# Optimization experiments

Hardware: AMD Instinct MI355X
Metric: run time of the kernel (lower is better)

Reference implementation:

```python
import jax, jax.numpy as jnp
import numpy as np

NUM_GRAPHS = 4096
EPS = 1e-6

def _ln(x, g, b):
    mu = jnp.mean(x, axis=-1, keepdims=True)
    var = jnp.mean(jnp.square(x - mu), axis=-1, keepdims=True)
    return (x - mu) * jax.lax.rsqrt(var + EPS) * g + b

def setup_inputs() -> dict:
    key = jax.random.key(0)
    ks = jax.random.split(key, 8)
    N, D, H, DRUG = 262144, 128, 8, 128
    feat = jax.random.normal(ks[0], (N, D), dtype=jnp.float32)
    batch = jnp.sort(jax.random.randint(ks[1], (N,), 0, NUM_GRAPHS)).astype(jnp.int64)
    def lin(k, fi, fo):
        lim = 1.0 / np.sqrt(fi)
        return jax.random.uniform(k, (fi, fo), jnp.float32, -lim, lim)
    return {
        'feat': feat, 'batch': batch,
        'W1': lin(ks[2], D, 64), 'b1': jnp.zeros((64,), jnp.float32),
        'g1': jnp.ones((64,), jnp.float32), 'beta1': jnp.zeros((64,), jnp.float32),
        'W2': lin(ks[3], 64, H), 'b2': jnp.zeros((H,), jnp.float32),
        'W3': lin(ks[4], H * D, D), 'b3': jnp.zeros((D,), jnp.float32),
        'g3': jnp.ones((D,), jnp.float32), 'beta3': jnp.zeros((D,), jnp.float32),
        'W4': lin(ks[5], D, DRUG), 'b4': jnp.zeros((DRUG,), jnp.float32),
        'g4': jnp.ones((DRUG,), jnp.float32), 'beta4': jnp.zeros((DRUG,), jnp.float32),
    }

def reference(feat, batch, W1, b1, g1, beta1, W2, b2, W3, b3, g3, beta3, W4, b4, g4, beta4):
    seg = batch.astype(jnp.int32)
    # ATFC: Linear -> LeakyReLU -> LayerNorm -> Linear
    h = jax.nn.leaky_relu(feat @ W1 + b1)
    h = _ln(h, g1, beta1)
    att = jnp.exp(h @ W2 + b2)                      # [N, H]
    # segment softmax normalization
    s = jax.ops.segment_sum(att, seg, num_segments=NUM_GRAPHS)  # [B, H]
    att = att / s[seg]
    # weighted aggregation: outer product + segment sum -> [B, H, D]
    out = jax.ops.segment_sum(att[:, :, None] * feat[:, None, :], seg, num_segments=NUM_GRAPHS)
    out = out.reshape(NUM_GRAPHS, -1)               # [B, H*D]
    # output block (dropout is identity in eval mode)
    o = _ln(jax.nn.leaky_relu(out @ W3 + b3), g3, beta3)
    o = _ln(jax.nn.leaky_relu(o @ W4 + b4), g4, beta4)
    return o
```

## Files before the change

kernel.cpp:

```cpp
#include <hip/hip_runtime.h>
#include <math.h>

#define NG 4096
#define NN 262144
#define D 128
#define M1 64
#define NH 8
#define GPB 8
#define EPS 1e-6f

typedef __attribute__((ext_vector_type(8))) short short8;
typedef __attribute__((ext_vector_type(8))) unsigned char uchar8;
typedef __attribute__((ext_vector_type(4))) float f32x4;

__device__ inline float leaky(float x) { return x > 0.f ? x : 0.01f * x; }

__device__ inline short f2bf(float f) {
  union { float f; unsigned u; } v; v.f = f;
  unsigned r = (v.u + 0x7fffu + ((v.u >> 16) & 1u)) >> 16;
  return (short)r;
}
__device__ inline float bf2f(short s) {
  union { unsigned u; float f; } v;
  v.u = ((unsigned)(unsigned short)s) << 16;
  return v.f;
}

__global__ __launch_bounds__(256) void k0b_prep(
    const float* __restrict__ W3, const float* __restrict__ W4,
    const int* __restrict__ batch,
    short* __restrict__ W3T, short* __restrict__ W4T,
    int* __restrict__ starts) {
  __shared__ float tile[64][65];
  int b = blockIdx.x, t = threadIdx.x;
  if (b >= 36) {
    int g = (b - 36) * 256 + t;
    int lo = 0, hi = NN;
    while (lo < hi) {
      int mid = (lo + hi) >> 1;
      if (batch[mid] < g) lo = mid + 1; else hi = mid;
    }
    starts[g] = lo;
    if (g == 0) starts[NG] = NN;
    return;
  }
  const float* src; short* dst; int kt, nt, tkl;
  if (b < 32) { src = W3; dst = W3T; kt = b >> 1; nt = b & 1; tkl = 1024; }
  else        { src = W4; dst = W4T; kt = (b - 32) >> 1; nt = (b - 32) & 1; tkl = 128; }

#pragma unroll
  for (int i = 0; i < 4; ++i) {
    int id = t + 256 * i;
    int r = id >> 4, c4 = (id & 15) * 4;
    float4 v = *(const float4*)(src + (size_t)(kt * 64 + r) * D + nt * 64 + c4);
    tile[r][c4 + 0] = v.x; tile[r][c4 + 1] = v.y;
    tile[r][c4 + 2] = v.z; tile[r][c4 + 3] = v.w;
  }
  __syncthreads();
  int n = t >> 2, kb = (t & 3) * 16;
  short8 p0, p1;
#pragma unroll
  for (int j = 0; j < 8; ++j) {
    p0[j] = f2bf(tile[kb + j][n]);
    p1[j] = f2bf(tile[kb + 8 + j][n]);
  }
  short* o = dst + (size_t)(nt * 64 + n) * tkl + kt * 64 + kb;
  *(short8*)o = p0;
  *(short8*)(o + 8) = p1;
}

__global__ __launch_bounds__(256, 2) void k_fused(
    const float* __restrict__ feat, const int* __restrict__ batch,
    const int* __restrict__ starts,
    const float* __restrict__ W1, const float* __restrict__ b1,
    const float* __restrict__ g1, const float* __restrict__ beta1,
    const float* __restrict__ W2, const float* __restrict__ b2,
    const short* __restrict__ W3T, const float* __restrict__ b3,
    const float* __restrict__ g3, const float* __restrict__ beta3,
    const short* __restrict__ W4T, const float* __restrict__ b4,
    const float* __restrict__ g4, const float* __restrict__ beta4,
    float* __restrict__ out) {
  __shared__ short W1T[M1][D + 8];
  __shared__ short W2T[16][M1 + 8];
  __shared__ short hb[128][72];
  __shared__ float agg[GPB][NH][D + 4];
  __shared__ float sL[GPB][NH];
  __shared__ unsigned char giL2[2][128];
  __shared__ float red[4][2][16];
  __shared__ short hbuf2[16][136];

  short (*attB)[136] = (short(*)[136])&hb[0][0];
  short (*aL)[1040] = (short(*)[1040])&hb[0][0];

  int t = threadIdx.x;
  int G0 = blockIdx.x * GPB;
  int w = t >> 6, l = t & 63;
  int lr = l & 15, lq = l >> 4;

#pragma unroll
  for (int i = 0; i < 8; ++i) {
    int idx4 = t + 256 * i;
    int k = idx4 >> 4, j = (idx4 & 15) * 4;
    float4 wv = *(const float4*)(W1 + k * M1 + j);
    W1T[j + 0][k] = f2bf(wv.x);
    W1T[j + 1][k] = f2bf(wv.y);
    W1T[j + 2][k] = f2bf(wv.z);
    W1T[j + 3][k] = f2bf(wv.w);
  }
#pragma unroll
  for (int i = 0; i < 4; ++i) {
    int e = t * 4 + i;
    int hh = e >> 6, j = e & 63;
    W2T[hh][j] = (hh < NH) ? f2bf(W2[j * NH + hh]) : (short)0;
  }
  for (int i = t; i < GPB * NH * (D + 4); i += 256) (&agg[0][0][0])[i] = 0.f;
  if (t < GPB * NH) (&sL[0][0])[t] = 0.f;

  float b1v[4], g1v[4], btv[4];
#pragma unroll
  for (int nt = 0; nt < 4; ++nt) {
    b1v[nt] = b1[nt * 16 + lr];
    g1v[nt] = g1[nt * 16 + lr];
    btv[nt] = beta1[nt * 16 + lr];
  }
  float b2v = b2[lr & 7];

  int s0 = starts[G0], s1 = starts[G0 + GPB];
  int nchunks = (s1 - s0 + 127) >> 7;

  for (int c = 0; c < nchunks; ++c) {
    int base = s0 + (c << 7);
    int nvalid = min(128, s1 - base);
    unsigned char* gi = giL2[c & 1];
    if (t < 128)
      gi[t] = (t < nvalid) ? (unsigned char)(batch[base + t] - G0)
                           : (unsigned char)255;

    short8 afr[2][4];
#pragma unroll
    for (int mt = 0; mt < 2; ++mt) {
      int node = base + w * 32 + mt * 16 + lr;
      node = node < NN ? node : NN - 1;
      const float* rp = feat + (size_t)node * D + lq * 8;
#pragma unroll
      for (int cc = 0; cc < 4; ++cc) {
        float4 x0 = *(const float4*)(rp + cc * 32);
        float4 x1 = *(const float4*)(rp + cc * 32 + 4);
        short8 a;
        a[0] = f2bf(x0.x); a[1] = f2bf(x0.y); a[2] = f2bf(x0.z); a[3] = f2bf(x0.w);
        a[4] = f2bf(x1.x); a[5] = f2bf(x1.y); a[6] = f2bf(x1.z); a[7] = f2bf(x1.w);
        afr[mt][cc] = a;
      }
    }
    __syncthreads();

    f32x4 acc[2][4];
#pragma unroll
    for (int mt = 0; mt < 2; ++mt)
#pragma unroll
      for (int nt = 0; nt < 4; ++nt) acc[mt][nt] = (f32x4){0.f, 0.f, 0.f, 0.f};
#pragma unroll
    for (int cc = 0; cc < 4; ++cc) {
#pragma unroll
      for (int nt = 0; nt < 4; ++nt) {
        short8 bfr = *(const short8*)&W1T[nt * 16 + lr][cc * 32 + lq * 8];
        acc[0][nt] = __builtin_amdgcn_mfma_f32_16x16x32_bf16(afr[0][cc], bfr, acc[0][nt], 0, 0, 0);
        acc[1][nt] = __builtin_amdgcn_mfma_f32_16x16x32_bf16(afr[1][cc], bfr, acc[1][nt], 0, 0, 0);
      }
    }

#pragma unroll
    for (int mt = 0; mt < 2; ++mt) {
#pragma unroll
      for (int r = 0; r < 4; ++r) {
        float x[4], sa = 0.f, sb = 0.f;
#pragma unroll
        for (int nt = 0; nt < 4; ++nt) {
          float xvv = leaky(acc[mt][nt][r] + b1v[nt]);
          x[nt] = xvv; sa += xvv; sb = fmaf(xvv, xvv, sb);
        }
#pragma unroll
        for (int off = 1; off < 16; off <<= 1) {
          sa += __shfl_xor(sa, off);
          sb += __shfl_xor(sb, off);
        }
        float mu = sa * (1.f / M1);
        float var = sb * (1.f / M1) - mu * mu;
        float inv = rsqrtf(var + EPS);
        int node = w * 32 + mt * 16 + lq * 4 + r;
#pragma unroll
        for (int nt = 0; nt < 4; ++nt)
          hb[node][nt * 16 + lr] = f2bf((x[nt] - mu) * inv * g1v[nt] + btv[nt]);
      }
    }
    __syncthreads();

    f32x4 acc2[2];
    acc2[0] = (f32x4){0.f, 0.f, 0.f, 0.f};
    acc2[1] = (f32x4){0.f, 0.f, 0.f, 0.f};
#pragma unroll
    for (int c2 = 0; c2 < 2; ++c2) {
      short8 bfr2 = *(const short8*)&W2T[lr][c2 * 32 + lq * 8];
#pragma unroll
      for (int mt = 0; mt < 2; ++mt) {
        short8 af2 = *(const short8*)&hb[w * 32 + mt * 16 + lr][c2 * 32 + lq * 8];
        acc2[mt] = __builtin_amdgcn_mfma_f32_16x16x32_bf16(af2, bfr2, acc2[mt], 0, 0, 0);
      }
    }
    __syncthreads();

    int gl_lo = gi[0];
    int gl_hi = gi[nvalid - 1];

    if (lr < NH) {
      float attv[2][4];
      int gnode[2][4];
#pragma unroll
      for (int mt = 0; mt < 2; ++mt)
#pragma unroll
        for (int r = 0; r < 4; ++r) {
          int node = w * 32 + mt * 16 + lq * 4 + r;
          float av = bf2f(f2bf(expf(acc2[mt][r] + b2v)));
          attv[mt][r] = av;
          gnode[mt][r] = gi[node];
          attB[lr][node] = f2bf(av);
        }
      for (int g = gl_lo; g <= gl_hi; ++g) {
        float ss = 0.f;
#pragma unroll
        for (int mt = 0; mt < 2; ++mt)
#pragma unroll
          for (int r = 0; r < 4; ++r)
            ss += (gnode[mt][r] == g) ? attv[mt][r] : 0.f;
        ss += __shfl_xor(ss, 16);
        ss += __shfl_xor(ss, 32);
        if (lq == 0) atomicAdd(&sL[g][lr], ss);
      }
    }
    __syncthreads();

    int dA = w * 32 + lr, dB = dA + 16;
    short8 bfA[4], bfB[4];
#pragma unroll
    for (int kc = 0; kc < 4; ++kc) {
      short8 ba, bb;
#pragma unroll
      for (int j = 0; j < 8; ++j) {
        int node = base + kc * 32 + lq * 8 + j;
        node = node < NN ? node : NN - 1;
        const float* fp = feat + (size_t)node * D;
        ba[j] = f2bf(fp[dA]);
        bb[j] = f2bf(fp[dB]);
      }
      bfA[kc] = ba;
      bfB[kc] = bb;
    }

    int hA = lr & 7;
    for (int gp = gl_lo; gp <= gl_hi; gp += 4) {
      int t0 = gp + (lr >> 3);
      int t1 = t0 + 2;
      f32x4 c00 = (f32x4){0.f, 0.f, 0.f, 0.f};
      f32x4 c01 = (f32x4){0.f, 0.f, 0.f, 0.f};
      f32x4 c10 = (f32x4){0.f, 0.f, 0.f, 0.f};
      f32x4 c11 = (f32x4){0.f, 0.f, 0.f, 0.f};
#pragma unroll
      for (int kc = 0; kc < 4; ++kc) {
        short8 av = *(const short8*)&attB[hA][kc * 32 + lq * 8];
        uchar8 gv = *(const uchar8*)&gi[kc * 32 + lq * 8];
        short8 a0, a1;
#pragma unroll
        for (int j = 0; j < 8; ++j) {
          short x = av[j];
          a0[j] = (gv[j] == t0) ? x : (short)0;
          a1[j] = (gv[j] == t1) ? x : (short)0;
        }
        c00 = __builtin_amdgcn_mfma_f32_16x16x32_bf16(a0, bfA[kc], c00, 0, 0, 0);
        c01 = __builtin_amdgcn_mfma_f32_16x16x32_bf16(a0, bfB[kc], c01, 0, 0, 0);
        c10 = __builtin_amdgcn_mfma_f32_16x16x32_bf16(a1, bfA[kc], c10, 0, 0, 0);
        c11 = __builtin_amdgcn_mfma_f32_16x16x32_bf16(a1, bfB[kc], c11, 0, 0, 0);
      }
      int giC0 = gp + (lq >> 1);
      int giC1 = giC0 + 2;
      int hC = (lq & 1) * 4;
      if (giC0 < GPB) {
#pragma unroll
        for (int r = 0; r < 4; ++r) {
          agg[giC0][hC + r][dA] += c00[r];
          agg[giC0][hC + r][dB] += c01[r];
        }
      }
      if (giC1 < GPB) {
#pragma unroll
        for (int r = 0; r < 4; ++r) {
          agg[giC1][hC + r][dA] += c10[r];
          agg[giC1][hC + r][dB] += c11[r];
        }
      }
    }
  }
  __syncthreads();

  if (t < GPB * NH) {
    float sv = (&sL[0][0])[t];
    (&sL[0][0])[t] = sv > 0.f ? 1.f / sv : 0.f;
  }
  __syncthreads();

  for (int i = t; i < GPB * NH * D; i += 256) {
    int gi2 = i >> 10;
    int k = i & 1023;
    int h = k >> 7, d = k & 127;
    aL[gi2][k] = f2bf(agg[gi2][h][d] * sL[gi2][h]);
  }
  __syncthreads();

  int ar = lr & 7;
  f32x4 acc3[2];
  acc3[0] = (f32x4){0.f, 0.f, 0.f, 0.f};
  acc3[1] = (f32x4){0.f, 0.f, 0.f, 0.f};
#pragma unroll
  for (int kc = 0; kc < 32; ++kc) {
    short8 a = *(const short8*)&aL[ar][kc * 32 + lq * 8];
#pragma unroll
    for (int nt = 0; nt < 2; ++nt) {
      int ncol = w * 32 + nt * 16 + lr;
      short8 b = *(const short8*)(W3T + (size_t)ncol * 1024 + kc * 32 + lq * 8);
      acc3[nt] = __builtin_amdgcn_mfma_f32_16x16x32_bf16(a, b, acc3[nt], 0, 0, 0);
    }
  }

  float xv[2][4], sa[4] = {0.f, 0.f, 0.f, 0.f}, sb[4] = {0.f, 0.f, 0.f, 0.f};
#pragma unroll
  for (int nt = 0; nt < 2; ++nt) {
    float bb = b3[w * 32 + nt * 16 + lr];
#pragma unroll
    for (int r = 0; r < 4; ++r) {
      float v = leaky(acc3[nt][r] + bb);
      xv[nt][r] = v;
      sa[r] += v;
      sb[r] = fmaf(v, v, sb[r]);
    }
  }
#pragma unroll
  for (int off = 1; off < 16; off <<= 1)
#pragma unroll
    for (int r = 0; r < 4; ++r) {
      sa[r] += __shfl_xor(sa[r], off);
      sb[r] += __shfl_xor(sb[r], off);
    }
  if (lr == 0)
#pragma unroll
    for (int r = 0; r < 4; ++r) {
      red[w][0][lq * 4 + r] = sa[r];
      red[w][1][lq * 4 + r] = sb[r];
    }
  __syncthreads();
#pragma unroll
  for (int nt = 0; nt < 2; ++nt) {
    int col = w * 32 + nt * 16 + lr;
    float gg = g3[col], bt = beta3[col];
#pragma unroll
    for (int r = 0; r < 4; ++r) {
      int row = lq * 4 + r;
      float S1 = red[0][0][row] + red[1][0][row] + red[2][0][row] + red[3][0][row];
      float S2 = red[0][1][row] + red[1][1][row] + red[2][1][row] + red[3][1][row];
      float mu = S1 * (1.f / D);
      float var = S2 * (1.f / D) - mu * mu;
      float inv = rsqrtf(var + EPS);
      hbuf2[row][col] = f2bf((xv[nt][r] - mu) * inv * gg + bt);
    }
  }
  __syncthreads();

  f32x4 acc4[2];
  acc4[0] = (f32x4){0.f, 0.f, 0.f, 0.f};
  acc4[1] = (f32x4){0.f, 0.f, 0.f, 0.f};
#pragma unroll
  for (int kc = 0; kc < 4; ++kc) {
    short8 a2 = *(const short8*)&hbuf2[lr][kc * 32 + lq * 8];
#pragma unroll
    for (int nt = 0; nt < 2; ++nt) {
      int ncol = w * 32 + nt * 16 + lr;
      short8 b4f = *(const short8*)(W4T + (size_t)ncol * 128 + kc * 32 + lq * 8);
      acc4[nt] = __builtin_amdgcn_mfma_f32_16x16x32_bf16(a2, b4f, acc4[nt], 0, 0, 0);
    }
  }
#pragma unroll
  for (int r = 0; r < 4; ++r) { sa[r] = 0.f; sb[r] = 0.f; }
#pragma unroll
  for (int nt = 0; nt < 2; ++nt) {
    float bb = b4[w * 32 + nt * 16 + lr];
#pragma unroll
    for (int r = 0; r < 4; ++r) {
      float v = leaky(acc4[nt][r] + bb);
      xv[nt][r] = v;
      sa[r] += v;
      sb[r] = fmaf(v, v, sb[r]);
    }
  }
#pragma unroll
  for (int off = 1; off < 16; off <<= 1)
#pragma unroll
    for (int r = 0; r < 4; ++r) {
      sa[r] += __shfl_xor(sa[r], off);
      sb[r] += __shfl_xor(sb[r], off);
    }
  if (lr == 0)
#pragma unroll
    for (int r = 0; r < 4; ++r) {
      red[w][0][lq * 4 + r] = sa[r];
      red[w][1][lq * 4 + r] = sb[r];
    }
  __syncthreads();
#pragma unroll
  for (int nt = 0; nt < 2; ++nt) {
    int col = w * 32 + nt * 16 + lr;
    float gg = g4[col], bt = beta4[col];
#pragma unroll
    for (int r = 0; r < 4; ++r) {
      int row = lq * 4 + r;
      if (row < GPB) {
        float S1 = red[0][0][row] + red[1][0][row] + red[2][0][row] + red[3][0][row];
        float S2 = red[0][1][row] + red[1][1][row] + red[2][1][row] + red[3][1][row];
        float mu = S1 * (1.f / D);
        float var = S2 * (1.f / D) - mu * mu;
        float inv = rsqrtf(var + EPS);
        out[(size_t)(G0 + row) * D + col] = (xv[nt][r] - mu) * inv * gg + bt;
      }
    }
  }
}

extern "C" void kernel_launch(void* const* d_in, const int* in_sizes, int n_in,
                              void* d_out, int out_size, void* d_ws, size_t ws_size,
                              hipStream_t stream) {
  (void)in_sizes; (void)n_in; (void)out_size; (void)ws_size;
  const float* feat  = (const float*)d_in[0];
  const int*   batch = (const int*)d_in[1];
  const float* W1    = (const float*)d_in[2];
  const float* b1    = (const float*)d_in[3];
  const float* g1    = (const float*)d_in[4];
  const float* beta1 = (const float*)d_in[5];
  const float* W2    = (const float*)d_in[6];
  const float* b2    = (const float*)d_in[7];
  const float* W3    = (const float*)d_in[8];
  const float* b3    = (const float*)d_in[9];
  const float* g3    = (const float*)d_in[10];
  const float* beta3 = (const float*)d_in[11];
  const float* W4    = (const float*)d_in[12];
  const float* b4    = (const float*)d_in[13];
  const float* g4    = (const float*)d_in[14];
  const float* beta4 = (const float*)d_in[15];
  float* out = (float*)d_out;

  char* ws = (char*)d_ws;
  short* W3T   = (short*)ws;
  short* W4T   = (short*)(ws + 262144);
  int*  starts = (int*)(ws + 262144 + 32768);

  k0b_prep<<<52, 256, 0, stream>>>(W3, W4, batch, W3T, W4T, starts);
  k_fused<<<NG / GPB, 256, 0, stream>>>(feat, batch, starts, W1, b1, g1, beta1,
                                        W2, b2, W3T, b3, g3, beta3, W4T, b4, g4,
                                        beta4, out);
}
```

Measured before the change: 268.0 us.

## Halve graphs per block, keep aggregation in MFMA registers, overlay shared memory

Each block now handles 4 graphs instead of 8, so the segment-aggregation accumulators fit in four persistent MFMA register tiles across chunks. This removes the large shared-memory agg buffer and its read-modify-write traffic. Weight tiles and epilogue buffers share one shared-memory union, the strided feature gather is moved earlier to overlap the first matmul, and s_setprio hints are added around the MFMA loops. Launch bounds rise to 4 blocks per CU to raise occupancy, at the cost of twice as many blocks and more register pressure.

```diff
diff --git a/kernel.cpp b/kernel.cpp
--- a/kernel.cpp
+++ b/kernel.cpp
@@ -6,7 +6,7 @@
 #define D 128
 #define M1 64
 #define NH 8
-#define GPB 8
+#define GPB 4
 #define EPS 1e-6f
 
 typedef __attribute__((ext_vector_type(8))) short short8;
@@ -69,7 +69,7 @@
   *(short8*)(o + 8) = p1;
 }
 
-__global__ __launch_bounds__(256, 2) void k_fused(
+__global__ __launch_bounds__(256, 4) void k_fused(
     const float* __restrict__ feat, const int* __restrict__ batch,
     const int* __restrict__ starts,
     const float* __restrict__ W1, const float* __restrict__ b1,
@@ -80,40 +80,39 @@
     const short* __restrict__ W4T, const float* __restrict__ b4,
     const float* __restrict__ g4, const float* __restrict__ beta4,
     float* __restrict__ out) {
-  __shared__ short W1T[M1][D + 8];
-  __shared__ short W2T[16][M1 + 8];
-  __shared__ short hb[128][72];
-  __shared__ float agg[GPB][NH][D + 4];
+  __shared__ __align__(16) union SOvl {
+    struct { short W1T[M1][D + 8]; short W2T[16][M1 + 8]; } p;
+    struct { short hbuf2[16][136]; float red[4][2][16]; } e;
+  } ovl;
+  __shared__ __align__(16) short hb[128][72];
+  __shared__ __align__(16) short attB[NH][136];
   __shared__ float sL[GPB][NH];
   __shared__ unsigned char giL2[2][128];
-  __shared__ float red[4][2][16];
-  __shared__ short hbuf2[16][136];
-
-  short (*attB)[136] = (short(*)[136])&hb[0][0];
+
   short (*aL)[1040] = (short(*)[1040])&hb[0][0];
 
   int t = threadIdx.x;
   int G0 = blockIdx.x * GPB;
   int w = t >> 6, l = t & 63;
   int lr = l & 15, lq = l >> 4;
+  int dA = w * 32 + lr, dB = dA + 16;
 
 #pragma unroll
   for (int i = 0; i < 8; ++i) {
     int idx4 = t + 256 * i;
     int k = idx4 >> 4, j = (idx4 & 15) * 4;
     float4 wv = *(const float4*)(W1 + k * M1 + j);
-    W1T[j + 0][k] = f2bf(wv.x);
-    W1T[j + 1][k] = f2bf(wv.y);
-    W1T[j + 2][k] = f2bf(wv.z);
-    W1T[j + 3][k] = f2bf(wv.w);
+    ovl.p.W1T[j + 0][k] = f2bf(wv.x);
+    ovl.p.W1T[j + 1][k] = f2bf(wv.y);
+    ovl.p.W1T[j + 2][k] = f2bf(wv.z);
+    ovl.p.W1T[j + 3][k] = f2bf(wv.w);
   }
 #pragma unroll
   for (int i = 0; i < 4; ++i) {
     int e = t * 4 + i;
     int hh = e >> 6, j = e & 63;
-    W2T[hh][j] = (hh < NH) ? f2bf(W2[j * NH + hh]) : (short)0;
-  }
-  for (int i = t; i < GPB * NH * (D + 4); i += 256) (&agg[0][0][0])[i] = 0.f;
+    ovl.p.W2T[hh][j] = (hh < NH) ? f2bf(W2[j * NH + hh]) : (short)0;
+  }
   if (t < GPB * NH) (&sL[0][0])[t] = 0.f;
 
   float b1v[4], g1v[4], btv[4];
@@ -124,6 +123,11 @@
     btv[nt] = beta1[nt * 16 + lr];
   }
   float b2v = b2[lr & 7];
+
+  f32x4 c00 = (f32x4){0.f, 0.f, 0.f, 0.f};
+  f32x4 c01 = (f32x4){0.f, 0.f, 0.f, 0.f};
+  f32x4 c10 = (f32x4){0.f, 0.f, 0.f, 0.f};
+  f32x4 c11 = (f32x4){0.f, 0.f, 0.f, 0.f};
 
   int s0 = starts[G0], s1 = starts[G0 + GPB];
   int nchunks = (s1 - s0 + 127) >> 7;
@@ -152,6 +156,21 @@
         afr[mt][cc] = a;
       }
     }
+    short8 bfA[4], bfB[4];
+#pragma unroll
+    for (int kc = 0; kc < 4; ++kc) {
+      short8 ba, bb;
+#pragma unroll
+      for (int j = 0; j < 8; ++j) {
+        int node = base + kc * 32 + lq * 8 + j;
+        node = node < NN ? node : NN - 1;
+        const float* fp = feat + (size_t)node * D;
+        ba[j] = f2bf(fp[dA]);
+        bb[j] = f2bf(fp[dB]);
+      }
+      bfA[kc] = ba;
+      bfB[kc] = bb;
+    }
     __syncthreads();
 
     f32x4 acc[2][4];
@@ -159,15 +178,17 @@
     for (int mt = 0; mt < 2; ++mt)
 #pragma unroll
       for (int nt = 0; nt < 4; ++nt) acc[mt][nt] = (f32x4){0.f, 0.f, 0.f, 0.f};
+    __builtin_amdgcn_s_setprio(1);
 #pragma unroll
     for (int cc = 0; cc < 4; ++cc) {
 #pragma unroll
       for (int nt = 0; nt < 4; ++nt) {
-        short8 bfr = *(const short8*)&W1T[nt * 16 + lr][cc * 32 + lq * 8];
+        short8 bfr = *(const short8*)&ovl.p.W1T[nt * 16 + lr][cc * 32 + lq * 8];
         acc[0][nt] = __builtin_amdgcn_mfma_f32_16x16x32_bf16(afr[0][cc], bfr, acc[0][nt], 0, 0, 0);
         acc[1][nt] = __builtin_amdgcn_mfma_f32_16x16x32_bf16(afr[1][cc], bfr, acc[1][nt], 0, 0, 0);
       }
     }
+    __builtin_amdgcn_s_setprio(0);
 
 #pragma unroll
     for (int mt = 0; mt < 2; ++mt) {
@@ -200,14 +221,13 @@
     acc2[1] = (f32x4){0.f, 0.f, 0.f, 0.f};
 #pragma unroll
     for (int c2 = 0; c2 < 2; ++c2) {
-      short8 bfr2 = *(const short8*)&W2T[lr][c2 * 32 + lq * 8];
+      short8 bfr2 = *(const short8*)&ovl.p.W2T[lr][c2 * 32 + lq * 8];
 #pragma unroll
       for (int mt = 0; mt < 2; ++mt) {
         short8 af2 = *(const short8*)&hb[w * 32 + mt * 16 + lr][c2 * 32 + lq * 8];
         acc2[mt] = __builtin_amdgcn_mfma_f32_16x16x32_bf16(af2, bfr2, acc2[mt], 0, 0, 0);
       }
     }
-    __syncthreads();
 
     int gl_lo = gi[0];
     int gl_hi = gi[nvalid - 1];
@@ -239,65 +259,33 @@
     }
     __syncthreads();
 
-    int dA = w * 32 + lr, dB = dA + 16;
-    short8 bfA[4], bfB[4];
+    int hA = lr & 7;
+    int t0 = lr >> 3;
+    int t1 = t0 + 2;
+    __builtin_amdgcn_s_setprio(1);
 #pragma unroll
     for (int kc = 0; kc < 4; ++kc) {
-      short8 ba, bb;
-#pragma unroll
-      for (int j = 0; j < 8; ++j) {
-        int node = base + kc * 32 + lq * 8 + j;
-        node = node < NN ? node : NN - 1;
-        const float* fp = feat + (size_t)node * D;
-        ba[j] = f2bf(fp[dA]);
-        bb[j] = f2bf(fp[dB]);
-      }
-      bfA[kc] = ba;
-      bfB[kc] = bb;
-    }
-
-    int hA = lr & 7;
-    for (int gp = gl_lo; gp <= gl_hi; gp += 4) {
-      int t0 = gp + (lr >> 3);
-      int t1 = t0 + 2;
-      f32x4 c00 = (f32x4){0.f, 0.f, 0.f, 0.f};
-      f32x4 c01 = (f32x4){0.f, 0.f, 0.f, 0.f};
-      f32x4 c10 = (f32x4){0.f, 0.f, 0.f, 0.f};
-      f32x4 c11 = (f32x4){0.f, 0.f, 0.f, 0.f};
-#pragma unroll
-      for (int kc = 0; kc < 4; ++kc) {
-        short8 av = *(const short8*)&attB[hA][kc * 32 + lq * 8];
-        uchar8 gv = *(const uchar8*)&gi[kc * 32 + lq * 8];
-        short8 a0, a1;
-#pragma unroll
-        for (int j = 0; j < 8; ++j) {
-          short x = av[j];
-          a0[j] = (gv[j] == t0) ? x : (short)0;
-          a1[j] = (gv[j] == t1) ? x : (short)0;
-        }
+      int lo0 = gi[kc * 32];
+      if (lo0 > 3) continue;
+      int hi0 = gi[kc * 32 + 31];
+      short8 av = *(const short8*)&attB[hA][kc * 32 + lq * 8];
+      uchar8 gv = *(const uchar8*)&gi[kc * 32 + lq * 8];
+      if (lo0 <= 1) {
+        short8 a0;
+#pragma unroll
+        for (int j = 0; j < 8; ++j) a0[j] = (gv[j] == t0) ? av[j] : (short)0;
         c00 = __builtin_amdgcn_mfma_f32_16x16x32_bf16(a0, bfA[kc], c00, 0, 0, 0);
         c01 = __builtin_amdgcn_mfma_f32_16x16x32_bf16(a0, bfB[kc], c01, 0, 0, 0);
+      }
+      if (hi0 >= 2) {
+        short8 a1;
+#pragma unroll
+        for (int j = 0; j < 8; ++j) a1[j] = (gv[j] == t1) ? av[j] : (short)0;
         c10 = __builtin_amdgcn_mfma_f32_16x16x32_bf16(a1, bfA[kc], c10, 0, 0, 0);
         c11 = __builtin_amdgcn_mfma_f32_16x16x32_bf16(a1, bfB[kc], c11, 0, 0, 0);
       }
-      int giC0 = gp + (lq >> 1);
-      int giC1 = giC0 + 2;
-      int hC = (lq & 1) * 4;
-      if (giC0 < GPB) {
-#pragma unroll
-        for (int r = 0; r < 4; ++r) {
-          agg[giC0][hC + r][dA] += c00[r];
-          agg[giC0][hC + r][dB] += c01[r];
-        }
-      }
-      if (giC1 < GPB) {
-#pragma unroll
-        for (int r = 0; r < 4; ++r) {
-          agg[giC1][hC + r][dA] += c10[r];
-          agg[giC1][hC + r][dB] += c11[r];
-        }
-      }
-    }
+    }
+    __builtin_amdgcn_s_setprio(0);
   }
   __syncthreads();
 
@@ -307,15 +295,21 @@
   }
   __syncthreads();
 
-  for (int i = t; i < GPB * NH * D; i += 256) {
-    int gi2 = i >> 10;
-    int k = i & 1023;
-    int h = k >> 7, d = k & 127;
-    aL[gi2][k] = f2bf(agg[gi2][h][d] * sL[gi2][h]);
-  }
-  __syncthreads();
-
-  int ar = lr & 7;
+  {
+    int g0 = lq >> 1, g1i = g0 + 2;
+    int hC = (lq & 1) * 4;
+#pragma unroll
+    for (int r = 0; r < 4; ++r) {
+      float i0 = sL[g0][hC + r], i1 = sL[g1i][hC + r];
+      aL[g0][(hC + r) * 128 + dA] = f2bf(c00[r] * i0);
+      aL[g0][(hC + r) * 128 + dB] = f2bf(c01[r] * i0);
+      aL[g1i][(hC + r) * 128 + dA] = f2bf(c10[r] * i1);
+      aL[g1i][(hC + r) * 128 + dB] = f2bf(c11[r] * i1);
+    }
+  }
+  __syncthreads();
+
+  int ar = lr & 3;
   f32x4 acc3[2];
   acc3[0] = (f32x4){0.f, 0.f, 0.f, 0.f};
   acc3[1] = (f32x4){0.f, 0.f, 0.f, 0.f};
@@ -352,8 +346,8 @@
   if (lr == 0)
 #pragma unroll
     for (int r = 0; r < 4; ++r) {
-      red[w][0][lq * 4 + r] = sa[r];
-      red[w][1][lq * 4 + r] = sb[r];
+      ovl.e.red[w][0][lq * 4 + r] = sa[r];
+      ovl.e.red[w][1][lq * 4 + r] = sb[r];
     }
   __syncthreads();
 #pragma unroll
@@ -363,12 +357,14 @@
 #pragma unroll
     for (int r = 0; r < 4; ++r) {
       int row = lq * 4 + r;
-      float S1 = red[0][0][row] + red[1][0][row] + red[2][0][row] + red[3][0][row];
-      float S2 = red[0][1][row] + red[1][1][row] + red[2][1][row] + red[3][1][row];
+      float S1 = ovl.e.red[0][0][row] + ovl.e.red[1][0][row] +
+                 ovl.e.red[2][0][row] + ovl.e.red[3][0][row];
+      float S2 = ovl.e.red[0][1][row] + ovl.e.red[1][1][row] +
+                 ovl.e.red[2][1][row] + ovl.e.red[3][1][row];
       float mu = S1 * (1.f / D);
       float var = S2 * (1.f / D) - mu * mu;
       float inv = rsqrtf(var + EPS);
-      hbuf2[row][col] = f2bf((xv[nt][r] - mu) * inv * gg + bt);
+      ovl.e.hbuf2[row][col] = f2bf((xv[nt][r] - mu) * inv * gg + bt);
     }
   }
   __syncthreads();
@@ -378,7 +374,7 @@
   acc4[1] = (f32x4){0.f, 0.f, 0.f, 0.f};
 #pragma unroll
   for (int kc = 0; kc < 4; ++kc) {
-    short8 a2 = *(const short8*)&hbuf2[lr][kc * 32 + lq * 8];
+    short8 a2 = *(const short8*)&ovl.e.hbuf2[lr][kc * 32 + lq * 8];
 #pragma unroll
     for (int nt = 0; nt < 2; ++nt) {
       int ncol = w * 32 + nt * 16 + lr;
@@ -406,11 +402,12 @@
       sa[r] += __shfl_xor(sa[r], off);
       sb[r] += __shfl_xor(sb[r], off);
     }
+  __syncthreads();
   if (lr == 0)
 #pragma unroll
     for (int r = 0; r < 4; ++r) {
-      red[w][0][lq * 4 + r] = sa[r];
-      red[w][1][lq * 4 + r] = sb[r];
+      ovl.e.red[w][0][lq * 4 + r] = sa[r];
+      ovl.e.red[w][1][lq * 4 + r] = sb[r];
     }
   __syncthreads();
 #pragma unroll
@@ -421,8 +418,10 @@
     for (int r = 0; r < 4; ++r) {
       int row = lq * 4 + r;
       if (row < GPB) {
-        float S1 = red[0][0][row] + red[1][0][row] + red[2][0][row] + red[3][0][row];
-        float S2 = red[0][1][row] + red[1][1][row] + red[2][1][row] + red[3][1][row];
+        float S1 = ovl.e.red[0][0][row] + ovl.e.red[1][0][row] +
+                   ovl.e.red[2][0][row] + ovl.e.red[3][0][row];
+        float S2 = ovl.e.red[0][1][row] + ovl.e.red[1][1][row] +
+                   ovl.e.red[2][1][row] + ovl.e.red[3][1][row];
         float mu = S1 * (1.f / D);
         float var = S2 * (1.f / D) - mu * mu;
         float inv = rsqrtf(var + EPS);
```

Result: slower. 385.2 us (+43.8%).

## Split fused kernel into node-parallel attention and graph-parallel aggregation kernels

Applied to the files above, without the earlier changes.

The single fused kernel is split in two. The first is node-parallel, with one block per 128 nodes: it computes the attention logits, writes bf16 attention transposed to global memory, and atomically accumulates per-graph softmax sums. The second is graph-parallel: it re-reads feat and attention to build the per-graph aggregation with masked MFMA accumulators kept in registers rather than LDS atomics, then runs the output MLP. This removes the serial per-block chunk loop and the LDS agg buffer, which should improve occupancy, but it reads feat twice, adds global atomics and a memset, and adds an extra launch.

```diff
diff --git a/kernel.cpp b/kernel.cpp
--- a/kernel.cpp
+++ b/kernel.cpp
@@ -10,7 +10,7 @@
 #define EPS 1e-6f
 
 typedef __attribute__((ext_vector_type(8))) short short8;
-typedef __attribute__((ext_vector_type(8))) unsigned char uchar8;
+typedef __attribute__((ext_vector_type(4))) short short4v;
 typedef __attribute__((ext_vector_type(4))) float f32x4;
 
 __device__ inline float leaky(float x) { return x > 0.f ? x : 0.01f * x; }
@@ -69,31 +69,20 @@
   *(short8*)(o + 8) = p1;
 }
 
-__global__ __launch_bounds__(256, 2) void k_fused(
+__global__ __launch_bounds__(256, 2) void kA_att(
     const float* __restrict__ feat, const int* __restrict__ batch,
-    const int* __restrict__ starts,
     const float* __restrict__ W1, const float* __restrict__ b1,
     const float* __restrict__ g1, const float* __restrict__ beta1,
     const float* __restrict__ W2, const float* __restrict__ b2,
-    const short* __restrict__ W3T, const float* __restrict__ b3,
-    const float* __restrict__ g3, const float* __restrict__ beta3,
-    const short* __restrict__ W4T, const float* __restrict__ b4,
-    const float* __restrict__ g4, const float* __restrict__ beta4,
-    float* __restrict__ out) {
-  __shared__ short W1T[M1][D + 8];
-  __shared__ short W2T[16][M1 + 8];
-  __shared__ short hb[128][72];
-  __shared__ float agg[GPB][NH][D + 4];
-  __shared__ float sL[GPB][NH];
-  __shared__ unsigned char giL2[2][128];
-  __shared__ float red[4][2][16];
-  __shared__ short hbuf2[16][136];
-
-  short (*attB)[136] = (short(*)[136])&hb[0][0];
-  short (*aL)[1040] = (short(*)[1040])&hb[0][0];
+    short* __restrict__ attT, float* __restrict__ s_sum) {
+  __shared__ __align__(16) short W1T[M1][D + 8];
+  __shared__ __align__(16) short W2T[16][M1 + 8];
+  __shared__ __align__(16) short hb[128][72];
+  __shared__ __align__(16) short attB[NH][136];
+  __shared__ int batchL[128];
 
   int t = threadIdx.x;
-  int G0 = blockIdx.x * GPB;
+  int nb = blockIdx.x * 128;
   int w = t >> 6, l = t & 63;
   int lr = l & 15, lq = l >> 4;
 
@@ -113,8 +102,7 @@
     int hh = e >> 6, j = e & 63;
     W2T[hh][j] = (hh < NH) ? f2bf(W2[j * NH + hh]) : (short)0;
   }
-  for (int i = t; i < GPB * NH * (D + 4); i += 256) (&agg[0][0][0])[i] = 0.f;
-  if (t < GPB * NH) (&sL[0][0])[t] = 0.f;
+  if (t < 128) batchL[t] = batch[nb + t];
 
   float b1v[4], g1v[4], btv[4];
 #pragma unroll
@@ -125,193 +113,216 @@
   }
   float b2v = b2[lr & 7];
 
+  short8 afr[2][4];
+#pragma unroll
+  for (int mt = 0; mt < 2; ++mt) {
+    const float* rp = feat + (size_t)(nb + w * 32 + mt * 16 + lr) * D + lq * 8;
+#pragma unroll
+    for (int cc = 0; cc < 4; ++cc) {
+      float4 x0 = *(const float4*)(rp + cc * 32);
+      float4 x1 = *(const float4*)(rp + cc * 32 + 4);
+      short8 a;
+      a[0] = f2bf(x0.x); a[1] = f2bf(x0.y); a[2] = f2bf(x0.z); a[3] = f2bf(x0.w);
+      a[4] = f2bf(x1.x); a[5] = f2bf(x1.y); a[6] = f2bf(x1.z); a[7] = f2bf(x1.w);
+      afr[mt][cc] = a;
+    }
+  }
+  __syncthreads();
+
+  f32x4 acc[2][4];
+#pragma unroll
+  for (int mt = 0; mt < 2; ++mt)
+#pragma unroll
+    for (int nt = 0; nt < 4; ++nt) acc[mt][nt] = (f32x4){0.f, 0.f, 0.f, 0.f};
+  __builtin_amdgcn_s_setprio(1);
+#pragma unroll
+  for (int cc = 0; cc < 4; ++cc) {
+#pragma unroll
+    for (int nt = 0; nt < 4; ++nt) {
+      short8 bfr = *(const short8*)&W1T[nt * 16 + lr][cc * 32 + lq * 8];
+      acc[0][nt] = __builtin_amdgcn_mfma_f32_16x16x32_bf16(afr[0][cc], bfr, acc[0][nt], 0, 0, 0);
+      acc[1][nt] = __builtin_amdgcn_mfma_f32_16x16x32_bf16(afr[1][cc], bfr, acc[1][nt], 0, 0, 0);
+    }
+  }
+  __builtin_amdgcn_s_setprio(0);
+
+#pragma unroll
+  for (int mt = 0; mt < 2; ++mt) {
+#pragma unroll
+    for (int r = 0; r < 4; ++r) {
+      float x[4], sa = 0.f, sb = 0.f;
+#pragma unroll
+      for (int nt = 0; nt < 4; ++nt) {
+        float xvv = leaky(acc[mt][nt][r] + b1v[nt]);
+        x[nt] = xvv; sa += xvv; sb = fmaf(xvv, xvv, sb);
+      }
+#pragma unroll
+      for (int off = 1; off < 16; off <<= 1) {
+        sa += __shfl_xor(sa, off);
+        sb += __shfl_xor(sb, off);
+      }
+      float mu = sa * (1.f / M1);
+      float var = sb * (1.f / M1) - mu * mu;
+      float inv = rsqrtf(var + EPS);
+      int node = w * 32 + mt * 16 + lq * 4 + r;
+#pragma unroll
+      for (int nt = 0; nt < 4; ++nt)
+        hb[node][nt * 16 + lr] = f2bf((x[nt] - mu) * inv * g1v[nt] + btv[nt]);
+    }
+  }
+  __syncthreads();
+
+  f32x4 acc2[2];
+  acc2[0] = (f32x4){0.f, 0.f, 0.f, 0.f};
+  acc2[1] = (f32x4){0.f, 0.f, 0.f, 0.f};
+#pragma unroll
+  for (int c2 = 0; c2 < 2; ++c2) {
+    short8 bfr2 = *(const short8*)&W2T[lr][c2 * 32 + lq * 8];
+#pragma unroll
+    for (int mt = 0; mt < 2; ++mt) {
+      short8 af2 = *(const short8*)&hb[w * 32 + mt * 16 + lr][c2 * 32 + lq * 8];
+      acc2[mt] = __builtin_amdgcn_mfma_f32_16x16x32_bf16(af2, bfr2, acc2[mt], 0, 0, 0);
+    }
+  }
+
+  int g_lo = batchL[0], g_hi = batchL[127];
+
+  if (lr < NH) {
+    float attv[2][4];
+    int bnode[2][4];
+#pragma unroll
+    for (int mt = 0; mt < 2; ++mt)
+#pragma unroll
+      for (int r = 0; r < 4; ++r) {
+        int node = w * 32 + mt * 16 + lq * 4 + r;
+        float av = bf2f(f2bf(expf(acc2[mt][r] + b2v)));
+        attv[mt][r] = av;
+        bnode[mt][r] = batchL[node];
+        attB[lr][node] = f2bf(av);
+      }
+    for (int g = g_lo; g <= g_hi; ++g) {
+      float ss = 0.f;
+#pragma unroll
+      for (int mt = 0; mt < 2; ++mt)
+#pragma unroll
+        for (int r = 0; r < 4; ++r)
+          ss += (bnode[mt][r] == g) ? attv[mt][r] : 0.f;
+      ss += __shfl_xor(ss, 16);
+      ss += __shfl_xor(ss, 32);
+      if (lq == 0) atomicAdd(s_sum + g * NH + lr, ss);
+    }
+  }
+  __syncthreads();
+
+  {
+    int h = t >> 5, c4 = (t & 31) * 4;
+    short4v v = *(const short4v*)&attB[h][c4];
+    *(short4v*)(attT + (size_t)h * NN + nb + c4) = v;
+  }
+}
+
+__global__ __launch_bounds__(256, 2) void kB_agg(
+    const float* __restrict__ feat, const int* __restrict__ batch,
+    const int* __restrict__ starts, const short* __restrict__ attT,
+    const float* __restrict__ s_sum,
+    const short* __restrict__ W3T, const float* __restrict__ b3,
+    const float* __restrict__ g3, const float* __restrict__ beta3,
+    const short* __restrict__ W4T, const float* __restrict__ b4,
+    const float* __restrict__ g4, const float* __restrict__ beta4,
+    float* __restrict__ out) {
+  __shared__ __align__(16) short aLb[GPB][1040];
+  __shared__ __align__(16) short hbuf2[16][136];
+  __shared__ float red[4][2][16];
+  __shared__ float sLb[GPB * NH];
+
+  int t = threadIdx.x;
+  int G0 = blockIdx.x * GPB;
+  int w = t >> 6, l = t & 63;
+  int lr = l & 15, lq = l >> 4;
+  int dA = w * 32 + lr, dB = dA + 16;
+  int hA = lr & 7;
+  int laneoff = lr >> 3;
+
   int s0 = starts[G0], s1 = starts[G0 + GPB];
-  int nchunks = (s1 - s0 + 127) >> 7;
-
-  for (int c = 0; c < nchunks; ++c) {
-    int base = s0 + (c << 7);
-    int nvalid = min(128, s1 - base);
-    unsigned char* gi = giL2[c & 1];
-    if (t < 128)
-      gi[t] = (t < nvalid) ? (unsigned char)(batch[base + t] - G0)
-                           : (unsigned char)255;
-
-    short8 afr[2][4];
-#pragma unroll
-    for (int mt = 0; mt < 2; ++mt) {
-      int node = base + w * 32 + mt * 16 + lr;
-      node = node < NN ? node : NN - 1;
-      const float* rp = feat + (size_t)node * D + lq * 8;
-#pragma unroll
-      for (int cc = 0; cc < 4; ++cc) {
-        float4 x0 = *(const float4*)(rp + cc * 32);
-        float4 x1 = *(const float4*)(rp + cc * 32 + 4);
-        short8 a;
-        a[0] = f2bf(x0.x); a[1] = f2bf(x0.y); a[2] = f2bf(x0.z); a[3] = f2bf(x0.w);
-        a[4] = f2bf(x1.x); a[5] = f2bf(x1.y); a[6] = f2bf(x1.z); a[7] = f2bf(x1.w);
-        afr[mt][cc] = a;
-      }
-    }
-    __syncthreads();
-
-    f32x4 acc[2][4];
-#pragma unroll
-    for (int mt = 0; mt < 2; ++mt)
-#pragma unroll
-      for (int nt = 0; nt < 4; ++nt) acc[mt][nt] = (f32x4){0.f, 0.f, 0.f, 0.f};
-#pragma unroll
-    for (int cc = 0; cc < 4; ++cc) {
-#pragma unroll
-      for (int nt = 0; nt < 4; ++nt) {
-        short8 bfr = *(const short8*)&W1T[nt * 16 + lr][cc * 32 + lq * 8];
-        acc[0][nt] = __builtin_amdgcn_mfma_f32_16x16x32_bf16(afr[0][cc], bfr, acc[0][nt], 0, 0, 0);
-        acc[1][nt] = __builtin_amdgcn_mfma_f32_16x16x32_bf16(afr[1][cc], bfr, acc[1][nt], 0, 0, 0);
-      }
-    }
-
-#pragma unroll
-    for (int mt = 0; mt < 2; ++mt) {
-#pragma unroll
-      for (int r = 0; r < 4; ++r) {
-        float x[4], sa = 0.f, sb = 0.f;
-#pragma unroll
-        for (int nt = 0; nt < 4; ++nt) {
-          float xvv = leaky(acc[mt][nt][r] + b1v[nt]);
-          x[nt] = xvv; sa += xvv; sb = fmaf(xvv, xvv, sb);
+  int base0 = s0 & ~127;
+  int nch = (s1 - base0 + 127) >> 7;
+
+  f32x4 cc[4][2];
+#pragma unroll
+  for (int T = 0; T < 4; ++T) {
+    cc[T][0] = (f32x4){0.f, 0.f, 0.f, 0.f};
+    cc[T][1] = (f32x4){0.f, 0.f, 0.f, 0.f};
+  }
+
+  for (int c = 0; c < nch; ++c) {
+    int base = base0 + (c << 7);
+    int lo0 = batch[base];
+    int hi0 = batch[min(base + 127, NN - 1)];
+    if (hi0 < G0 || lo0 > G0 + GPB - 1) continue;
+    bool fastp = (base + 128 <= NN);
+#pragma unroll 1
+    for (int kc = 0; kc < 4; ++kc) {
+      int nb0 = base + kc * 32;
+      int klo = batch[min(nb0, NN - 1)];
+      int khi = batch[min(nb0 + 31, NN - 1)];
+      if (khi < G0 || klo > G0 + GPB - 1) continue;
+      int n0 = nb0 + lq * 8;
+      short8 av;
+      int bv[8];
+      short8 bfa, bfb;
+      if (fastp) {
+        av = *(const short8*)(attT + (size_t)hA * NN + n0);
+        int4 bx = *(const int4*)(batch + n0);
+        int4 by = *(const int4*)(batch + n0 + 4);
+        bv[0] = bx.x; bv[1] = bx.y; bv[2] = bx.z; bv[3] = bx.w;
+        bv[4] = by.x; bv[5] = by.y; bv[6] = by.z; bv[7] = by.w;
+#pragma unroll
+        for (int j = 0; j < 8; ++j) {
+          const float* fp = feat + (size_t)(n0 + j) * D;
+          bfa[j] = f2bf(fp[dA]);
+          bfb[j] = f2bf(fp[dB]);
         }
-#pragma unroll
-        for (int off = 1; off < 16; off <<= 1) {
-          sa += __shfl_xor(sa, off);
-          sb += __shfl_xor(sb, off);
+      } else {
+#pragma unroll
+        for (int j = 0; j < 8; ++j) {
+          int n = min(n0 + j, NN - 1);
+          av[j] = attT[(size_t)hA * NN + n];
+          bv[j] = batch[n];
+          const float* fp = feat + (size_t)n * D;
+          bfa[j] = f2bf(fp[dA]);
+          bfb[j] = f2bf(fp[dB]);
         }
-        float mu = sa * (1.f / M1);
-        float var = sb * (1.f / M1) - mu * mu;
-        float inv = rsqrtf(var + EPS);
-        int node = w * 32 + mt * 16 + lq * 4 + r;
-#pragma unroll
-        for (int nt = 0; nt < 4; ++nt)
-          hb[node][nt * 16 + lr] = f2bf((x[nt] - mu) * inv * g1v[nt] + btv[nt]);
-      }
-    }
-    __syncthreads();
-
-    f32x4 acc2[2];
-    acc2[0] = (f32x4){0.f, 0.f, 0.f, 0.f};
-    acc2[1] = (f32x4){0.f, 0.f, 0.f, 0.f};
-#pragma unroll
-    for (int c2 = 0; c2 < 2; ++c2) {
-      short8 bfr2 = *(const short8*)&W2T[lr][c2 * 32 + lq * 8];
-#pragma unroll
-      for (int mt = 0; mt < 2; ++mt) {
-        short8 af2 = *(const short8*)&hb[w * 32 + mt * 16 + lr][c2 * 32 + lq * 8];
-        acc2[mt] = __builtin_amdgcn_mfma_f32_16x16x32_bf16(af2, bfr2, acc2[mt], 0, 0, 0);
-      }
-    }
-    __syncthreads();
-
-    int gl_lo = gi[0];
-    int gl_hi = gi[nvalid - 1];
-
-    if (lr < NH) {
-      float attv[2][4];
-      int gnode[2][4];
-#pragma unroll
-      for (int mt = 0; mt < 2; ++mt)
-#pragma unroll
-        for (int r = 0; r < 4; ++r) {
-          int node = w * 32 + mt * 16 + lq * 4 + r;
-          float av = bf2f(f2bf(expf(acc2[mt][r] + b2v)));
-          attv[mt][r] = av;
-          gnode[mt][r] = gi[node];
-          attB[lr][node] = f2bf(av);
-        }
-      for (int g = gl_lo; g <= gl_hi; ++g) {
-        float ss = 0.f;
-#pragma unroll
-        for (int mt = 0; mt < 2; ++mt)
-#pragma unroll
-          for (int r = 0; r < 4; ++r)
-            ss += (gnode[mt][r] == g) ? attv[mt][r] : 0.f;
-        ss += __shfl_xor(ss, 16);
-        ss += __shfl_xor(ss, 32);
-        if (lq == 0) atomicAdd(&sL[g][lr], ss);
-      }
-    }
-    __syncthreads();
-
-    int dA = w * 32 + lr, dB = dA + 16;
-    short8 bfA[4], bfB[4];
-#pragma unroll
-    for (int kc = 0; kc < 4; ++kc) {
-      short8 ba, bb;
-#pragma unroll
-      for (int j = 0; j < 8; ++j) {
-        int node = base + kc * 32 + lq * 8 + j;
-        node = node < NN ? node : NN - 1;
-        const float* fp = feat + (size_t)node * D;
-        ba[j] = f2bf(fp[dA]);
-        bb[j] = f2bf(fp[dB]);
-      }
-      bfA[kc] = ba;
-      bfB[kc] = bb;
-    }
-
-    int hA = lr & 7;
-    for (int gp = gl_lo; gp <= gl_hi; gp += 4) {
-      int t0 = gp + (lr >> 3);
-      int t1 = t0 + 2;
-      f32x4 c00 = (f32x4){0.f, 0.f, 0.f, 0.f};
-      f32x4 c01 = (f32x4){0.f, 0.f, 0.f, 0.f};
-      f32x4 c10 = (f32x4){0.f, 0.f, 0.f, 0.f};
-      f32x4 c11 = (f32x4){0.f, 0.f, 0.f, 0.f};
-#pragma unroll
-      for (int kc = 0; kc < 4; ++kc) {
-        short8 av = *(const short8*)&attB[hA][kc * 32 + lq * 8];
-        uchar8 gv = *(const uchar8*)&gi[kc * 32 + lq * 8];
-        short8 a0, a1;
-#pragma unroll
-        for (int j = 0; j < 8; ++j) {
-          short x = av[j];
-          a0[j] = (gv[j] == t0) ? x : (short)0;
-          a1[j] = (gv[j] == t1) ? x : (short)0;
-        }
-        c00 = __builtin_amdgcn_mfma_f32_16x16x32_bf16(a0, bfA[kc], c00, 0, 0, 0);
-        c01 = __builtin_amdgcn_mfma_f32_16x16x32_bf16(a0, bfB[kc], c01, 0, 0, 0);
-        c10 = __builtin_amdgcn_mfma_f32_16x16x32_bf16(a1, bfA[kc], c10, 0, 0, 0);
-        c11 = __builtin_amdgcn_mfma_f32_16x16x32_bf16(a1, bfB[kc], c11, 0, 0, 0);
-      }
-      int giC0 = gp + (lq >> 1);
-      int giC1 = giC0 + 2;
-      int hC = (lq & 1) * 4;
-      if (giC0 < GPB) {
-#pragma unroll
-        for (int r = 0; r < 4; ++r) {
-          agg[giC0][hC + r][dA] += c00[r];
-          agg[giC0][hC + r][dB] += c01[r];
-        }
-      }
-      if (giC1 < GPB) {
-#pragma unroll
-        for (int r = 0; r < 4; ++r) {
-          agg[giC1][hC + r][dA] += c10[r];
-          agg[giC1][hC + r][dB] += c11[r];
-        }
-      }
-    }
-  }
-  __syncthreads();
+      }
+#pragma unroll
+      for (int T = 0; T < 4; ++T) {
+        int tg = G0 + 2 * T;
+        if (khi < tg || klo > tg + 1) continue;
+        int tgt = tg + laneoff;
+        short8 am;
+#pragma unroll
+        for (int j = 0; j < 8; ++j) am[j] = (bv[j] == tgt) ? av[j] : (short)0;
+        cc[T][0] = __builtin_amdgcn_mfma_f32_16x16x32_bf16(am, bfa, cc[T][0], 0, 0, 0);
+        cc[T][1] = __builtin_amdgcn_mfma_f32_16x16x32_bf16(am, bfb, cc[T][1], 0, 0, 0);
+      }
+    }
+  }
 
   if (t < GPB * NH) {
-    float sv = (&sL[0][0])[t];
-    (&sL[0][0])[t] = sv > 0.f ? 1.f / sv : 0.f;
-  }
-  __syncthreads();
-
-  for (int i = t; i < GPB * NH * D; i += 256) {
-    int gi2 = i >> 10;
-    int k = i & 1023;
-    int h = k >> 7, d = k & 127;
-    aL[gi2][k] = f2bf(agg[gi2][h][d] * sL[gi2][h]);
+    float sv = s_sum[G0 * NH + t];
+    sLb[t] = sv > 0.f ? 1.f / sv : 0.f;
+  }
+  __syncthreads();
+
+#pragma unroll
+  for (int T = 0; T < 4; ++T) {
+    int gi = 2 * T + (lq >> 1);
+    int hC = (lq & 1) * 4;
+#pragma unroll
+    for (int r = 0; r < 4; ++r) {
+      float inv = sLb[gi * NH + hC + r];
+      aLb[gi][(hC + r) * 128 + dA] = f2bf(cc[T][0][r] * inv);
+      aLb[gi][(hC + r) * 128 + dB] = f2bf(cc[T][1][r] * inv);
+    }
   }
   __syncthreads();
 
@@ -321,7 +332,7 @@
   acc3[1] = (f32x4){0.f, 0.f, 0.f, 0.f};
 #pragma unroll
   for (int kc = 0; kc < 32; ++kc) {
-    short8 a = *(const short8*)&aL[ar][kc * 32 + lq * 8];
+    short8 a = *(const short8*)&aLb[ar][kc * 32 + lq * 8];
 #pragma unroll
     for (int nt = 0; nt < 2; ++nt) {
       int ncol = w * 32 + nt * 16 + lr;
@@ -406,6 +417,7 @@
       sa[r] += __shfl_xor(sa[r], off);
       sb[r] += __shfl_xor(sb[r], off);
     }
+  __syncthreads();
   if (lr == 0)
 #pragma unroll
     for (int r = 0; r < 4; ++r) {
@@ -455,12 +467,16 @@
   float* out = (float*)d_out;
 
   char* ws = (char*)d_ws;
-  short* W3T   = (short*)ws;
-  short* W4T   = (short*)(ws + 262144);
-  int*  starts = (int*)(ws + 262144 + 32768);
-
+  short* W3T    = (short*)ws;
+  short* W4T    = (short*)(ws + 262144);
+  int*   starts = (int*)(ws + 294912);
+  float* s_sum  = (float*)(ws + 311552);
+  short* attT   = (short*)(ws + 442624);
+
+  hipMemsetAsync(s_sum, 0, (size_t)NG * NH * 4, stream);
   k0b_prep<<<52, 256, 0, stream>>>(W3, W4, batch, W3T, W4T, starts);
-  k_fused<<<NG / GPB, 256, 0, stream>>>(feat, batch, starts, W1, b1, g1, beta1,
-                                        W2, b2, W3T, b3, g3, beta3, W4T, b4, g4,
-                                        beta4, out);
-}
+  kA_att<<<NN / 128, 256, 0, stream>>>(feat, batch, W1, b1, g1, beta1, W2, b2,
+                                       attT, s_sum);
+  kB_agg<<<NG / GPB, 256, 0, stream>>>(feat, batch, starts, attT, s_sum, W3T,
+                                       b3, g3, beta3, W4T, b4, g4, beta4, out);
+}
```

Result: slower. 279.6 us (+4.3%).
